# Performance work log

Measured on AMD Instinct MI355X. Metric: run time of the kernel, lower is better.

The kernel has to match this reference:

```python
import jax, jax.numpy as jnp
import numpy as np

N_S, N_G, D, K = 30000, 3000, 128, 16
SIGMA = 2.5
BOX = 60.0  # Angstrom box for random coordinates


def setup_inputs() -> dict:
    key = jax.random.key(0)
    ks = jax.random.split(key, 10)
    s = 1.0 / np.sqrt(D)
    return {
        'xs': jax.random.normal(ks[0], (N_S, D), jnp.float32),
        'xg': jax.random.normal(ks[1], (N_G, D), jnp.float32),
        'pos_s': jax.random.uniform(ks[2], (N_S, 3), jnp.float32) * BOX,
        'pos_g': jax.random.uniform(ks[3], (N_G, 3), jnp.float32) * BOX,
        'W_s_pre': jax.random.normal(ks[4], (D, D), jnp.float32) * s,
        'W_g_pre': jax.random.normal(ks[5], (D, D), jnp.float32) * s,
        'W_gs': jax.random.normal(ks[6], (D, D), jnp.float32) * s,
        'W_sg': jax.random.normal(ks[7], (D, D), jnp.float32) * s,
        'W_s_post': jax.random.normal(ks[8], (2 * D, D), jnp.float32) * s,
        'W_g_post': jax.random.normal(ks[9], (2 * D, D), jnp.float32) * s,
        'k': K,
    }


def reference(xs, xg, pos_s, pos_g, W_s_pre, W_g_pre, W_gs, W_sg, W_s_post, W_g_post, k):
    n_s, d = xs.shape
    # ---- compute_bipartite_graphs: knn of each graph node over surface nodes ----
    # squared pairwise distances via gemm form: (N_G, N_S)
    d2 = ((pos_g ** 2).sum(-1)[:, None] + (pos_s ** 2).sum(-1)[None, :]
          - 2.0 * pos_g @ pos_s.T)
    neg_d2, idx = jax.lax.top_k(-d2, k)          # idx: (N_G, K) surface neighbors
    w = jnp.exp(neg_d2 / (2.0 * SIGMA ** 2))     # RBF edge weight exp(-d^2/(2*sigma^2))
    # ---- pre blocks ----
    hs = xs @ W_s_pre                             # (N_S, D)
    hg = xg @ W_g_pre                             # (N_G, D)
    # ---- bp_gs block: graph -> surface weighted edge-conv (scatter-add) ----
    msg_gs = (hg @ W_gs)[:, None, :] * w[:, :, None]          # (N_G, K, D)
    xs_out = jnp.zeros((n_s, d), hs.dtype).at[idx.reshape(-1)].add(
        msg_gs.reshape(-1, d))
    # ---- bp_sg block: surface -> graph weighted edge-conv (gather-sum) ----
    xg_out = ((hs @ W_sg)[idx] * w[:, :, None]).sum(axis=1)   # (N_G, D)
    # ---- post blocks: combine pre features with message output ----
    xs_new = jax.nn.relu(jnp.concatenate([hs, xs_out], axis=-1) @ W_s_post)
    xg_new = jax.nn.relu(jnp.concatenate([hg, xg_out], axis=-1) @ W_g_post)
    return xs_new, xg_new
```

## Files before the change

kernel.cpp:

```cpp
#include <hip/hip_runtime.h>
#include <stdint.h>

#define N_S 30000
#define N_G 3000
#define DD  128
#define KK  16
#define NE  (N_G * KK)
#define NC  16
#define CELLS (NC * NC * NC)
#define CH  3.75f
#define CAP 16

#define FILL_BLOCKS 118
#define PACK_BLOCKS 384
#define KNN_BLOCKS  3000
#define NBS16 1875
#define NBG16 188
#define PRE_TILES (NBS16 + NBG16)
#define NBS 469
#define NBG 47
#define NTILE (NBS + NBG)

using v8s = __attribute__((ext_vector_type(8))) short;
using v4f = __attribute__((ext_vector_type(4))) float;

__device__ __forceinline__ float bf2f(unsigned short u) {
    union { unsigned int i; float f; } v; v.i = ((unsigned int)u) << 16; return v.f;
}
__device__ __forceinline__ unsigned short f2bf(float f) {
    union { float f; unsigned int i; } v; v.f = f;
    unsigned int x = v.i;
    return (unsigned short)((x + 0x7fffu + ((x >> 16) & 1u)) >> 16);
}
__device__ __forceinline__ float ldIn(const void* p, int i, int bf) {
    return bf ? bf2f(((const unsigned short*)p)[i]) : ((const float*)p)[i];
}
__device__ __forceinline__ void stOut(void* p, int i, float v, int bf) {
    if (bf) ((unsigned short*)p)[i] = f2bf(v);
    else    ((float*)p)[i] = v;
}
__device__ __forceinline__ int cellOf(float x) {
    int c = (int)(x * (1.0f / CH));
    if (c < 0) c = 0; if (c > NC - 1) c = NC - 1;
    return c;
}

__device__ __forceinline__ int detectFlag(const void* pos_g) {
    const unsigned int* w = (const unsigned int*)pos_g;
    int votes = 0;
#pragma unroll
    for (int i = 0; i < 16; ++i) {
        const unsigned int b = (w[i] >> 8) & 0xFFu;
        votes += (b >= 0x3Eu && b <= 0x42u) ? 1 : 0;
    }
    return votes >= 8;
}

__device__ void knn_node(int g, int bf, const void* pos_g,
                         const int* __restrict__ ccnt,
                         const float4* __restrict__ scell,
                         const float4* __restrict__ ovf, int novf,
                         int* __restrict__ idx_out, float* __restrict__ w_out,
                         unsigned short* map16, int* s_base, int* s_pref,
                         double* g_key, int* g_sid)
{
    const int t = threadIdx.x;

    const float gxf = ldIn(pos_g, 3 * g + 0, bf);
    const float gyf = ldIn(pos_g, 3 * g + 1, bf);
    const float gzf = ldIn(pos_g, 3 * g + 2, bf);
    const double gx = (double)gxf, gy = (double)gyf, gz = (double)gzf;
    const int cx = cellOf(gxf), cy = cellOf(gyf), cz = cellOf(gzf);

    double bk[KK]; int bi[KK];
#pragma unroll
    for (int j = 0; j < KK; ++j) { bk[j] = 1e300; bi[j] = 0x7fffffff; }

    bool inserted = false;

    for (int i = t; i < novf; i += 64) {
        const float4 cd = ovf[i];
        const double ddx = gx - (double)cd.x, ddy = gy - (double)cd.y, ddz = gz - (double)cd.z;
        const double d2 = ddx * ddx + ddy * ddy + ddz * ddz;
        const int sidx = __float_as_int(cd.w);
        if (d2 > bk[KK - 1] || (d2 == bk[KK - 1] && sidx > bi[KK - 1])) continue;
        inserted = true;
        double ck = d2; int ci2 = sidx;
#pragma unroll
        for (int j = 0; j < KK; ++j) {
            const bool less = (ck < bk[j]) || (ck == bk[j] && ci2 < bi[j]);
            const double nk = less ? ck : bk[j]; const int ni = less ? ci2 : bi[j];
            const double ok = less ? bk[j] : ck; const int oi = less ? bi[j] : ci2;
            bk[j] = nk; bi[j] = ni; ck = ok; ci2 = oi;
        }
    }

    double gk15 = 1e300;
    for (int R = 1; R <= NC; ++R) {
        const int S = 2 * R + 1;
        const int Scells = S * S * S;
        for (int cb = 0; cb < Scells; cb += 64) {
            const int ci = cb + t;
            int cnt = 0, base = 0;
            if (ci < Scells) {
                const int dz = ci % S - R;
                const int dy = (ci / S) % S - R;
                const int dx = ci / (S * S) - R;
                int ax = dx < 0 ? -dx : dx, ay = dy < 0 ? -dy : dy, az = dz < 0 ? -dz : dz;
                int cheb = ax > ay ? ax : ay; if (az > cheb) cheb = az;
                const bool want = (R == 1) ? true : (cheb == R);
                const int X = cx + dx, Y = cy + dy, Z = cz + dz;
                if (want && X >= 0 && X < NC && Y >= 0 && Y < NC && Z >= 0 && Z < NC) {
                    double m2c = 0.0;
                    {
                        const double lo = (double)X * 3.75, hi = lo + 3.75;
                        const double d = (gx < lo) ? (lo - gx) : ((gx > hi) ? (gx - hi) : 0.0);
                        m2c += d * d;
                    }
                    {
                        const double lo = (double)Y * 3.75, hi = lo + 3.75;
                        const double d = (gy < lo) ? (lo - gy) : ((gy > hi) ? (gy - hi) : 0.0);
                        m2c += d * d;
                    }
                    {
                        const double lo = (double)Z * 3.75, hi = lo + 3.75;
                        const double d = (gz < lo) ? (lo - gz) : ((gz > hi) ? (gz - hi) : 0.0);
                        m2c += d * d;
                    }
                    if (m2c <= gk15 * (1.0 + 1e-9) + 1e-300) {
                        const int cid = (X * NC + Y) * NC + Z;
                        int c = ccnt[cid]; if (c > CAP) c = CAP;
                        cnt = c; base = cid * CAP;
                    }
                }
            }
            int incl = cnt;
            for (int d = 1; d < 64; d <<= 1) {
                int v = __shfl_up(incl, d);
                if (t >= d) incl += v;
            }
            const int total = __shfl(incl, 63);
            const int pref = incl - cnt;
            s_base[t] = base; s_pref[t] = pref;
            for (int i = 0; i < cnt; ++i) map16[pref + i] = (unsigned short)t;
            __syncthreads();
            for (int pos = t; pos < total; pos += 64) {
                const int slot = map16[pos];
                const float4 cd = scell[s_base[slot] + (pos - s_pref[slot])];
                const double ddx = gx - (double)cd.x;
                const double ddy = gy - (double)cd.y;
                const double ddz = gz - (double)cd.z;
                const double d2 = ddx * ddx + ddy * ddy + ddz * ddz;
                const int sidx = __float_as_int(cd.w);
                if (d2 > bk[KK - 1]) continue;
                if (d2 == bk[KK - 1] && sidx > bi[KK - 1]) continue;
                inserted = true;
                double ck = d2; int ci2 = sidx;
#pragma unroll
                for (int j = 0; j < KK; ++j) {
                    const bool less = (ck < bk[j]) || (ck == bk[j] && ci2 < bi[j]);
                    const double nk = less ? ck : bk[j]; const int ni = less ? ci2 : bi[j];
                    const double ok = less ? bk[j] : ck; const int oi = less ? bi[j] : ci2;
                    bk[j] = nk; bi[j] = ni; ck = ok; ci2 = oi;
                }
            }
            __syncthreads();
        }
        if (__ballot(inserted) != 0ULL) {
            for (int p = 0; p < KK; ++p) {
                double key = bk[0]; int sid = bi[0];
                for (int d = 1; d < 64; d <<= 1) {
                    const double ok = __shfl_xor(key, d);
                    const int    os = __shfl_xor(sid, d);
                    if (ok < key || (ok == key && os < sid)) { key = ok; sid = os; }
                }
                if (t == 0) { g_key[p] = key; g_sid[p] = sid; }
                const bool win = (bk[0] == key) && (bi[0] == sid);
                if (win) {
#pragma unroll
                    for (int j = 0; j < KK - 1; ++j) { bk[j] = bk[j + 1]; bi[j] = bi[j + 1]; }
                    bk[KK - 1] = 1e300; bi[KK - 1] = 0x7fffffff;
                }
            }
            __syncthreads();
            gk15 = g_key[KK - 1];
            if (t == 0) {
#pragma unroll
                for (int j = 0; j < KK; ++j) { bk[j] = g_key[j]; bi[j] = g_sid[j]; }
            } else {
#pragma unroll
                for (int j = 0; j < KK; ++j) { bk[j] = 1e300; bi[j] = 0x7fffffff; }
            }
            __syncthreads();
            inserted = false;
        }
        double m = 1e300;
        if (cx - R > 0)      { double d = gx - (double)(cx - R) * 3.75; if (d < m) m = d; }
        if (cx + R < NC - 1) { double d = (double)(cx + R + 1) * 3.75 - gx; if (d < m) m = d; }
        if (cy - R > 0)      { double d = gy - (double)(cy - R) * 3.75; if (d < m) m = d; }
        if (cy + R < NC - 1) { double d = (double)(cy + R + 1) * 3.75 - gy; if (d < m) m = d; }
        if (cz - R > 0)      { double d = gz - (double)(cz - R) * 3.75; if (d < m) m = d; }
        if (cz + R < NC - 1) { double d = (double)(cz + R + 1) * 3.75 - gz; if (d < m) m = d; }
        if (m < 0.0) m = 0.0;
        const double m2 = m * m * (1.0 - 1e-12);
        if (gk15 < m2) break;
    }

    if (t == 0) {
        for (int p = 0; p < KK; ++p) {
            idx_out[g * KK + p] = g_sid[p];
            w_out[g * KK + p] = expf((float)(-g_key[p]) * (1.0f / 12.5f));
        }
    }
}

__device__ __forceinline__ v8s loadA_bf16(const unsigned short* p) {
    return *(const v8s*)p;
}
__device__ __forceinline__ v8s loadA_f32v(const float* f) {
    const float4 a = *(const float4*)f;
    const float4 b = *(const float4*)(f + 4);
    v8s r;
    r[0] = (short)f2bf(a.x); r[1] = (short)f2bf(a.y);
    r[2] = (short)f2bf(a.z); r[3] = (short)f2bf(a.w);
    r[4] = (short)f2bf(b.x); r[5] = (short)f2bf(b.y);
    r[6] = (short)f2bf(b.z); r[7] = (short)f2bf(b.w);
    return r;
}
__device__ __forceinline__ v8s loadA_raw(const void* A, size_t off, int bf) {
    if (bf) return loadA_bf16((const unsigned short*)A + off);
    return loadA_f32v((const float*)A + off);
}

__device__ void pre_tile16(int task, int bf, const void* xs, const void* xg,
                           const unsigned short* __restrict__ wpk_ps,
                           const unsigned short* __restrict__ wpk_pg,
                           unsigned short* __restrict__ hsb,
                           unsigned short* __restrict__ hgb,
                           float* __restrict__ xs_agg)
{
    const void* A; const unsigned short* wpk; unsigned short* outp; int M, m0;
    const bool is_s = (task < NBS16);
    if (is_s) { A = xs; wpk = wpk_ps; outp = hsb; M = N_S; m0 = task * 16; }
    else      { A = xg; wpk = wpk_pg; outp = hgb; M = N_G; m0 = (task - NBS16) * 16; }

    const int lane = threadIdx.x;
    const int q = lane >> 4, lm = lane & 15;
    const int mrow = m0 + lm;
    const bool valid = (mrow < M);

    v4f acc[8];
#pragma unroll
    for (int t = 0; t < 8; ++t) acc[t] = {0.f, 0.f, 0.f, 0.f};
    for (int ks = 0; ks < 4; ++ks) {
        v8s a = {0,0,0,0,0,0,0,0};
        if (valid) a = loadA_raw(A, (size_t)mrow * 128 + ks * 32 + q * 8, bf);
        const unsigned short* wb = wpk + (size_t)(ks * 4 + q) * 128 * 8;
#pragma unroll
        for (int t = 0; t < 8; ++t) {
            const v8s bfr = *(const v8s*)(wb + (t * 16 + lm) * 8);
            acc[t] = __builtin_amdgcn_mfma_f32_16x16x32_bf16(a, bfr, acc[t], 0, 0, 0);
        }
    }
#pragma unroll
    for (int t = 0; t < 8; ++t)
#pragma unroll
        for (int r = 0; r < 4; ++r) {
            const int row = m0 + q * 4 + r;
            if (row < M) outp[(size_t)row * 128 + t * 16 + lm] = f2bf(acc[t][r]);
        }
    if (is_s) {
        float4* dst = (float4*)(xs_agg + (size_t)m0 * 128);
        const float4 z = make_float4(0.f, 0.f, 0.f, 0.f);
        for (int i = lane; i < 16 * 32; i += 64) dst[i] = z;
    }
}

__device__ void post_tile(int task, int bf,
                          const unsigned short* __restrict__ hsb,
                          const float* __restrict__ xs_agg,
                          const unsigned short* __restrict__ hgb,
                          const unsigned short* __restrict__ aggg,
                          const unsigned short* __restrict__ wpk_cs,
                          const unsigned short* __restrict__ wpk_cg,
                          void* out)
{
    const unsigned short* A1; const void* A2; int a2f32; const unsigned short* wpk;
    int M, m0, ooff;
    if (task < NBS) { A1 = hsb; A2 = xs_agg; a2f32 = 1; wpk = wpk_cs; M = N_S; m0 = task * 64; ooff = 0; }
    else { A1 = hgb; A2 = aggg; a2f32 = 0; wpk = wpk_cg; M = N_G; m0 = (task - NBS) * 64; ooff = N_S * DD; }

    const int wave = threadIdx.x >> 6, lane = threadIdx.x & 63;
    const int q = lane >> 4, lm = lane & 15;
    const int mb = m0 + wave * 16;
    const int mrow = mb + lm;
    const bool valid = (mrow < M);

    v4f acc[8];
#pragma unroll
    for (int t = 0; t < 8; ++t) acc[t] = {0.f, 0.f, 0.f, 0.f};
    for (int ks = 0; ks < 8; ++ks) {
        const int kk = ks * 32 + q * 8;
        v8s a = {0,0,0,0,0,0,0,0};
        if (valid) {
            if (kk < 128)      a = loadA_bf16(A1 + (size_t)mrow * 128 + kk);
            else if (a2f32)    a = loadA_f32v((const float*)A2 + (size_t)mrow * 128 + (kk - 128));
            else               a = loadA_bf16((const unsigned short*)A2 + (size_t)mrow * 128 + (kk - 128));
        }
        const unsigned short* wb = wpk + (size_t)(ks * 4 + q) * 128 * 8;
#pragma unroll
        for (int t = 0; t < 8; ++t) {
            const v8s bfr = *(const v8s*)(wb + (t * 16 + lm) * 8);
            acc[t] = __builtin_amdgcn_mfma_f32_16x16x32_bf16(a, bfr, acc[t], 0, 0, 0);
        }
    }
#pragma unroll
    for (int t = 0; t < 8; ++t)
#pragma unroll
        for (int r = 0; r < 4; ++r) {
            const int row = mb + q * 4 + r;
            if (row < M) {
                float v = acc[t][r];
                if (v < 0.f) v = 0.f;
                stOut(out, ooff + row * DD + t * 16 + lm, v, bf);
            }
        }
}

__global__ __launch_bounds__(256) void fill_pack_kernel(
    const void* pos_s, const void* pos_g,
    const void* Wsp, const void* Wgp, const void* Wgs, const void* Wsg,
    const void* Wspost, const void* Wgpost,
    int* __restrict__ ccnt, float4* __restrict__ scell,
    float4* __restrict__ ovf, int* __restrict__ novf,
    unsigned short* __restrict__ wpk_ps, unsigned short* __restrict__ wpk_pg,
    unsigned short* __restrict__ wpk_cs, unsigned short* __restrict__ wpk_cg)
{
    const int bf = detectFlag(pos_g);
    const int bid = blockIdx.x, tid = threadIdx.x;
    if (bid < FILL_BLOCKS) {
        const int p = bid * 256 + tid;
        if (p < N_S) {
            const float x = ldIn(pos_s, 3 * p + 0, bf);
            const float y = ldIn(pos_s, 3 * p + 1, bf);
            const float z = ldIn(pos_s, 3 * p + 2, bf);
            const int cid = (cellOf(x) * NC + cellOf(y)) * NC + cellOf(z);
            const int slot = atomicAdd(&ccnt[cid], 1);
            const float4 pt = make_float4(x, y, z, __int_as_float(p));
            if (slot < CAP) scell[cid * CAP + slot] = pt;
            else            ovf[atomicAdd(novf, 1)] = pt;
        }
        return;
    }
    __shared__ float rows[256];
    const int rt = bid - FILL_BLOCKS;
    const int half = tid >> 7, j = tid & 127;
    const int task = rt * 2 + half;
    float v; unsigned short* dst; int k;
    if (task < 128) { k = task; v = ldIn(Wsp, k * DD + j, bf); dst = wpk_ps; }
    else if (task < 256) { k = task - 128; v = ldIn(Wgp, k * DD + j, bf); dst = wpk_pg; }
    else {
        const int which_g = (task >= 512);
        const int r = which_g ? (task - 512) : (task - 256);
        const void* W1 = which_g ? Wsg : Wgs;
        const void* Wp = which_g ? Wgpost : Wspost;
        dst = which_g ? wpk_cg : wpk_cs;
        k = r;
        if (r < 128) v = ldIn(Wp, r * DD + j, bf);
        else {
            rows[half * 128 + j] = ldIn(W1, (r - 128) * DD + j, bf);
            __syncthreads();
            float acc = 0.f;
            for (int m = 0; m < DD; ++m)
                acc += rows[half * 128 + m] * ldIn(Wp, (DD + m) * DD + j, bf);
            v = acc;
        }
    }
    const int ks = k >> 5, q = (k >> 3) & 3, i = k & 7;
    dst[((ks * 4 + q) * 128 + j) * 8 + i] = f2bf(v);
}

__global__ __launch_bounds__(64) void knn_pre_kernel(
    const void* xs, const void* xg, const void* pos_g,
    const int* __restrict__ ccnt, const float4* __restrict__ scell,
    const float4* __restrict__ ovf, const int* __restrict__ novf,
    int* __restrict__ idx, float* __restrict__ w,
    const unsigned short* __restrict__ wpk_ps,
    const unsigned short* __restrict__ wpk_pg,
    unsigned short* __restrict__ hsb, unsigned short* __restrict__ hgb,
    float* __restrict__ xs_agg)
{
    const int bf = detectFlag(pos_g);
    const int bid = blockIdx.x;
    if (bid < KNN_BLOCKS) {
        __shared__ unsigned short map16[64 * CAP];
        __shared__ int s_base[64];
        __shared__ int s_pref[64];
        __shared__ double g_key[KK];
        __shared__ int g_sid[KK];
        knn_node(bid, bf, pos_g, ccnt, scell, ovf, *novf, idx, w,
                 map16, s_base, s_pref, g_key, g_sid);
    } else {
        pre_tile16(bid - KNN_BLOCKS, bf, xs, xg, wpk_ps, wpk_pg, hsb, hgb, xs_agg);
    }
}

__global__ __launch_bounds__(256) void scatgath_kernel(
    const unsigned short* __restrict__ hsb, const unsigned short* __restrict__ hgb,
    const int* __restrict__ idx, const float* __restrict__ w,
    float* __restrict__ xs_agg, unsigned short* __restrict__ aggg)
{
    const int g = blockIdx.x;
    const int half = threadIdx.x >> 7, j = threadIdx.x & 127;
    if (half == 0) {
        const float m = bf2f(hgb[g * DD + j]);
#pragma unroll
        for (int k = 0; k < KK; ++k)
            atomicAdd(&xs_agg[(size_t)idx[g * KK + k] * DD + j], m * w[g * KK + k]);
    } else {
        float acc = 0.f;
#pragma unroll
        for (int k = 0; k < KK; ++k)
            acc += w[g * KK + k] * bf2f(hsb[(size_t)idx[g * KK + k] * DD + j]);
        aggg[g * DD + j] = f2bf(acc);
    }
}

__global__ __launch_bounds__(256) void mfma_post_kernel(
    const void* pos_g,
    const unsigned short* __restrict__ hsb, const float* __restrict__ xs_agg,
    const unsigned short* __restrict__ hgb, const unsigned short* __restrict__ aggg,
    const unsigned short* __restrict__ wpk_cs, const unsigned short* __restrict__ wpk_cg,
    void* out)
{
    const int bf = detectFlag(pos_g);
    post_tile(blockIdx.x, bf, hsb, xs_agg, hgb, aggg, wpk_cs, wpk_cg, out);
}

extern "C" void kernel_launch(void* const* d_in, const int* in_sizes, int n_in,
                              void* d_out, int out_size, void* d_ws, size_t ws_size,
                              hipStream_t stream)
{
    const void* xs       = d_in[0];
    const void* xg       = d_in[1];
    const void* pos_s    = d_in[2];
    const void* pos_g    = d_in[3];
    const void* W_s_pre  = d_in[4];
    const void* W_g_pre  = d_in[5];
    const void* W_gs     = d_in[6];
    const void* W_sg     = d_in[7];
    const void* W_s_post = d_in[8];
    const void* W_g_post = d_in[9];
    (void)in_sizes; (void)n_in; (void)out_size; (void)ws_size;

    char* ws = (char*)d_ws;
    size_t off_b = 0;
    auto alloc = [&](size_t bytes) -> void* {
        void* p = ws + off_b;
        off_b = (off_b + bytes + 255) & ~((size_t)255);
        return p;
    };
    unsigned short* hsb    = (unsigned short*)alloc((size_t)N_S * DD * 2);
    unsigned short* hgb    = (unsigned short*)alloc((size_t)N_G * DD * 2);
    unsigned short* aggg   = (unsigned short*)alloc((size_t)N_G * DD * 2);
    float*          xs_agg = (float*) alloc((size_t)N_S * DD * 4);
    unsigned short* wpk_ps = (unsigned short*)alloc((size_t)DD * DD * 2);
    unsigned short* wpk_pg = (unsigned short*)alloc((size_t)DD * DD * 2);
    unsigned short* wpk_cs = (unsigned short*)alloc((size_t)2 * DD * DD * 2);
    unsigned short* wpk_cg = (unsigned short*)alloc((size_t)2 * DD * DD * 2);
    int*            idx    = (int*)   alloc((size_t)NE * 4);
    float*          w      = (float*) alloc((size_t)NE * 4);
    int*            ccnt   = (int*)   alloc((size_t)CELLS * 4 + 4);
    int*            novf   = ccnt + CELLS;
    float4*         scell  = (float4*)alloc((size_t)CELLS * CAP * 16);
    float4*         ovf    = (float4*)alloc((size_t)N_S * 16);

    hipMemsetAsync(ccnt, 0, (size_t)CELLS * 4 + 4, stream);

    fill_pack_kernel<<<FILL_BLOCKS + PACK_BLOCKS, 256, 0, stream>>>(
        pos_s, pos_g, W_s_pre, W_g_pre, W_gs, W_sg, W_s_post, W_g_post,
        ccnt, scell, ovf, novf, wpk_ps, wpk_pg, wpk_cs, wpk_cg);

    knn_pre_kernel<<<KNN_BLOCKS + PRE_TILES, 64, 0, stream>>>(
        xs, xg, pos_g, ccnt, scell, ovf, novf, idx, w,
        wpk_ps, wpk_pg, hsb, hgb, xs_agg);

    scatgath_kernel<<<N_G, 256, 0, stream>>>(hsb, hgb, idx, w,
                                             xs_agg, aggg);

    mfma_post_kernel<<<NTILE, 256, 0, stream>>>(pos_g, hsb, xs_agg, hgb, aggg,
                                                wpk_cs, wpk_cg, d_out);
}
```

Measured before the change: 194.8 us.

## Add single-pass 3x3x3-cell kNN fast path with rank-based selection

Adds a fast kNN path that scans only the 27 neighbouring grid cells plus the overflow list. It compacts candidates closer than a guaranteed-safe radius into shared memory and picks the top-16 by counting ranks pairwise, with no per-thread insertion sort. If too few or too many candidates survive, it falls back to the original expanding-ring search, which now always does the cross-lane merge instead of checking an 'inserted' ballot. The goal is to cut the per-graph-node search cost in the kNN stage. The price is extra shared memory and a fallback path that may run more often than expected.

Result: no change. 191.8 us (-1.5%).

```diff
diff --git a/kernel.cpp b/kernel.cpp
--- a/kernel.cpp
+++ b/kernel.cpp
@@ -10,6 +10,7 @@
 #define CELLS (NC * NC * NC)
 #define CH  3.75f
 #define CAP 16
+#define SURV 192
 
 #define FILL_BLOCKS 118
 #define PACK_BLOCKS 384
@@ -56,6 +57,105 @@
     return votes >= 8;
 }
 
+__device__ bool knn_fast(int g, int bf, const void* pos_g,
+                         const int* __restrict__ ccnt,
+                         const float4* __restrict__ scell,
+                         const float4* __restrict__ ovf, int novf,
+                         int* __restrict__ idx_out, float* __restrict__ w_out,
+                         double* skey, int* ssid)
+{
+    const int t = threadIdx.x;
+
+    const float gxf = ldIn(pos_g, 3 * g + 0, bf);
+    const float gyf = ldIn(pos_g, 3 * g + 1, bf);
+    const float gzf = ldIn(pos_g, 3 * g + 2, bf);
+    const double gx = (double)gxf, gy = (double)gyf, gz = (double)gzf;
+    const int cx = cellOf(gxf), cy = cellOf(gyf), cz = cellOf(gzf);
+
+    double m = 1e300;
+    if (cx - 1 > 0)      { double d = gx - (double)(cx - 1) * 3.75; if (d < m) m = d; }
+    if (cx + 1 < NC - 1) { double d = (double)(cx + 2) * 3.75 - gx; if (d < m) m = d; }
+    if (cy - 1 > 0)      { double d = gy - (double)(cy - 1) * 3.75; if (d < m) m = d; }
+    if (cy + 1 < NC - 1) { double d = (double)(cy + 2) * 3.75 - gy; if (d < m) m = d; }
+    if (cz - 1 > 0)      { double d = gz - (double)(cz - 1) * 3.75; if (d < m) m = d; }
+    if (cz + 1 < NC - 1) { double d = (double)(cz + 2) * 3.75 - gz; if (d < m) m = d; }
+    if (m < 0.0) m = 0.0;
+    const double m2eff = (m < 1e299) ? m * m * (1.0 - 1e-12) : 1e300;
+
+    int cnt = 0, base = 0;
+    if (t < 27) {
+        const int dx = t / 9 - 1, dy = (t / 3) % 3 - 1, dz = t % 3 - 1;
+        const int X = cx + dx, Y = cy + dy, Z = cz + dz;
+        if (X >= 0 && X < NC && Y >= 0 && Y < NC && Z >= 0 && Z < NC) {
+            const int cid = (X * NC + Y) * NC + Z;
+            int c = ccnt[cid]; if (c > CAP) c = CAP;
+            cnt = c; base = cid * CAP;
+        }
+    }
+
+    int total = 0;
+    for (int i = 0; i < CAP; ++i) {
+        bool act = (i < cnt);
+        double d2 = 0.0; int sidx = 0;
+        if (act) {
+            const float4 cd = scell[base + i];
+            const double ddx = gx - (double)cd.x;
+            const double ddy = gy - (double)cd.y;
+            const double ddz = gz - (double)cd.z;
+            d2 = ddx * ddx + ddy * ddy + ddz * ddz;
+            sidx = __float_as_int(cd.w);
+            act = (d2 < m2eff);
+        }
+        const unsigned long long b = __ballot(act);
+        const int pos = total + __popcll(b & ((1ull << t) - 1ull));
+        if (act && pos < SURV) { skey[pos] = d2; ssid[pos] = sidx; }
+        total += (int)__popcll(b);
+    }
+    for (int i0 = 0; i0 < novf; i0 += 64) {
+        const int i = i0 + t;
+        bool act = (i < novf);
+        double d2 = 0.0; int sidx = 0;
+        if (act) {
+            const float4 cd = ovf[i];
+            const double ddx = gx - (double)cd.x;
+            const double ddy = gy - (double)cd.y;
+            const double ddz = gz - (double)cd.z;
+            d2 = ddx * ddx + ddy * ddy + ddz * ddz;
+            sidx = __float_as_int(cd.w);
+            act = (d2 < m2eff);
+        }
+        const unsigned long long b = __ballot(act);
+        const int pos = total + __popcll(b & ((1ull << t) - 1ull));
+        if (act && pos < SURV) { skey[pos] = d2; ssid[pos] = sidx; }
+        total += (int)__popcll(b);
+    }
+
+    if (total < KK || total > SURV) return false;
+    __syncthreads();
+
+    const int n = total;
+    double ki[3]; int si[3]; int rk[3]; int nv = 0;
+    for (int i = t; i < n; i += 64) {
+        ki[nv] = skey[i]; si[nv] = ssid[i]; rk[nv] = 0; ++nv;
+        if (nv == 3) break;
+    }
+    for (int j = 0; j < n; ++j) {
+        const double kj = skey[j]; const int sj = ssid[j];
+#pragma unroll
+        for (int q = 0; q < 3; ++q)
+            if (q < nv)
+                rk[q] += ((kj < ki[q]) || (kj == ki[q] && sj < si[q])) ? 1 : 0;
+    }
+#pragma unroll
+    for (int q = 0; q < 3; ++q) {
+        if (q < nv && rk[q] < KK) {
+            idx_out[g * KK + rk[q]] = si[q];
+            w_out[g * KK + rk[q]] = expf((float)(-ki[q]) * (1.0f / 12.5f));
+        }
+    }
+    return true;
+}
+
 __device__ void knn_node(int g, int bf, const void* pos_g,
                          const int* __restrict__ ccnt,
                          const float4* __restrict__ scell,
@@ -76,15 +176,12 @@
 #pragma unroll
     for (int j = 0; j < KK; ++j) { bk[j] = 1e300; bi[j] = 0x7fffffff; }
 
-    bool inserted = false;
-
     for (int i = t; i < novf; i += 64) {
         const float4 cd = ovf[i];
         const double ddx = gx - (double)cd.x, ddy = gy - (double)cd.y, ddz = gz - (double)cd.z;
         const double d2 = ddx * ddx + ddy * ddy + ddz * ddz;
         const int sidx = __float_as_int(cd.w);
         if (d2 > bk[KK - 1] || (d2 == bk[KK - 1] && sidx > bi[KK - 1])) continue;
-        inserted = true;
         double ck = d2; int ci2 = sidx;
 #pragma unroll
         for (int j = 0; j < KK; ++j) {
@@ -154,7 +251,6 @@
                 const int sidx = __float_as_int(cd.w);
                 if (d2 > bk[KK - 1]) continue;
                 if (d2 == bk[KK - 1] && sidx > bi[KK - 1]) continue;
-                inserted = true;
                 double ck = d2; int ci2 = sidx;
 #pragma unroll
                 for (int j = 0; j < KK; ++j) {
@@ -166,34 +262,31 @@
             }
             __syncthreads();
         }
-        if (__ballot(inserted) != 0ULL) {
-            for (int p = 0; p < KK; ++p) {
-                double key = bk[0]; int sid = bi[0];
-                for (int d = 1; d < 64; d <<= 1) {
-                    const double ok = __shfl_xor(key, d);
-                    const int    os = __shfl_xor(sid, d);
-                    if (ok < key || (ok == key && os < sid)) { key = ok; sid = os; }
-                }
-                if (t == 0) { g_key[p] = key; g_sid[p] = sid; }
-                const bool win = (bk[0] == key) && (bi[0] == sid);
-                if (win) {
-#pragma unroll
-                    for (int j = 0; j < KK - 1; ++j) { bk[j] = bk[j + 1]; bi[j] = bi[j + 1]; }
-                    bk[KK - 1] = 1e300; bi[KK - 1] = 0x7fffffff;
-                }
+        for (int p = 0; p < KK; ++p) {
+            double key = bk[0]; int sid = bi[0];
+            for (int d = 1; d < 64; d <<= 1) {
+                const double ok = __shfl_xor(key, d);
+                const int    os = __shfl_xor(sid, d);
+                if (ok < key || (ok == key && os < sid)) { key = ok; sid = os; }
             }
-            __syncthreads();
-            gk15 = g_key[KK - 1];
-            if (t == 0) {
-#pragma unroll
-                for (int j = 0; j < KK; ++j) { bk[j] = g_key[j]; bi[j] = g_sid[j]; }
-            } else {
-#pragma unroll
-                for (int j = 0; j < KK; ++j) { bk[j] = 1e300; bi[j] = 0x7fffffff; }
+            if (t == 0) { g_key[p] = key; g_sid[p] = sid; }
+            const bool win = (bk[0] == key) && (bi[0] == sid);
+            if (win) {
+#pragma unroll
+                for (int j = 0; j < KK - 1; ++j) { bk[j] = bk[j + 1]; bi[j] = bi[j + 1]; }
+                bk[KK - 1] = 1e300; bi[KK - 1] = 0x7fffffff;
             }
-            __syncthreads();
-            inserted = false;
-        }
+        }
+        __syncthreads();
+        gk15 = g_key[KK - 1];
+        if (t == 0) {
+#pragma unroll
+            for (int j = 0; j < KK; ++j) { bk[j] = g_key[j]; bi[j] = g_sid[j]; }
+        } else {
+#pragma unroll
+            for (int j = 0; j < KK; ++j) { bk[j] = 1e300; bi[j] = 0x7fffffff; }
+        }
+        __syncthreads();
         double m = 1e300;
         if (cx - R > 0)      { double d = gx - (double)(cx - R) * 3.75; if (d < m) m = d; }
         if (cx + R < NC - 1) { double d = (double)(cx + R + 1) * 3.75 - gx; if (d < m) m = d; }
@@ -393,13 +486,19 @@
     const int bf = detectFlag(pos_g);
     const int bid = blockIdx.x;
     if (bid < KNN_BLOCKS) {
-        __shared__ unsigned short map16[64 * CAP];
-        __shared__ int s_base[64];
-        __shared__ int s_pref[64];
-        __shared__ double g_key[KK];
-        __shared__ int g_sid[KK];
-        knn_node(bid, bf, pos_g, ccnt, scell, ovf, *novf, idx, w,
-                 map16, s_base, s_pref, g_key, g_sid);
+        __shared__ double skey[SURV];
+        __shared__ int    ssid[SURV];
+        const int nov = *novf;
+        if (!knn_fast(bid, bf, pos_g, ccnt, scell, ovf, nov, idx, w, skey, ssid)) {
+            __shared__ unsigned short map16[64 * CAP];
+            __shared__ int s_base[64];
+            __shared__ int s_pref[64];
+            __shared__ double g_key[KK];
+            __shared__ int g_sid[KK];
+            __syncthreads();
+            knn_node(bid, bf, pos_g, ccnt, scell, ovf, nov, idx, w,
+                     map16, s_base, s_pref, g_key, g_sid);
+        }
     } else {
         pre_tile16(bid - KNN_BLOCKS, bf, xs, xg, wpk_ps, wpk_pg, hsb, hgb, xs_agg);
     }
```
